# Kernel optimization log

Hardware: AMD Instinct MI355X
Metric: run time of the kernel (lower is better)

The kernel has to match this reference:

```python
import jax, jax.numpy as jnp
import numpy as np


def setup_inputs() -> dict:
    key = jax.random.key(0)
    k1, k2, k3, k4 = jax.random.split(key, 4)
    B, S, D, R = 8, 1024, 1024, 256
    batch = jax.random.normal(k1, (B, S, D), dtype=jnp.float32)
    proj_L = jax.random.uniform(k2, (D, R), dtype=jnp.float32, minval=-0.05, maxval=0.05)
    proj_R = jax.random.uniform(k3, (R, D), dtype=jnp.float32, minval=-0.05, maxval=0.05)
    bias = jax.random.uniform(k4, (1,), dtype=jnp.float32, minval=-0.05, maxval=0.05)
    return {"batch": batch, "proj_L": proj_L, "proj_R": proj_R, "bias": bias}


def reference(batch, proj_L, proj_R, bias):
    # logits[b,i,j] = h_i^T (L @ R) h_j + bias
    # Efficient factored form (same math, avoids O(B*S^2*D) intermediates):
    # left[b,i,r] = (batch @ L)[b,i,r]; right[b,j,r] = (batch @ R^T)[b,j,r]
    left = jnp.einsum('bid,dr->bir', batch, proj_L)    # (B,S,R)
    right = jnp.einsum('bjd,rd->bjr', batch, proj_R)   # (B,S,R)
    logits = jnp.einsum('bir,bjr->bij', left, right) + bias[0]
    return logits
```

## Files before the change

### kernel.cpp

```cpp
#include <hip/hip_runtime.h>

typedef __bf16 bf16_t;
typedef __bf16 bf16x8 __attribute__((ext_vector_type(8)));
typedef __bf16 bf16x4 __attribute__((ext_vector_type(4)));
typedef float f32x4 __attribute__((ext_vector_type(4)));

__device__ __forceinline__ void async16(const void* g, void* l) {
  __builtin_amdgcn_global_load_lds(
      (const __attribute__((address_space(1))) unsigned int*)g,
      (__attribute__((address_space(3))) unsigned int*)l,
      16, 0, 0);
}

__global__ void convert_f32_bf16(const float* __restrict__ in,
                                 bf16_t* __restrict__ out, int n4) {
  int i = blockIdx.x * blockDim.x + threadIdx.x;
  if (i >= n4) return;
  float4 v = ((const float4*)in)[i];
  bf16x4 o;
  o[0] = (bf16_t)v.x; o[1] = (bf16_t)v.y; o[2] = (bf16_t)v.z; o[3] = (bf16_t)v.w;
  ((bf16x4*)out)[i] = o;
}

__global__ void transpose_L(const float* __restrict__ in,
                            bf16_t* __restrict__ out) {
  __shared__ float tile[32][33];
  const int n0 = blockIdx.x * 32;
  const int k0 = blockIdx.y * 32;
  const int tx = threadIdx.x;
  const int ty = threadIdx.y;
#pragma unroll
  for (int i = 0; i < 32; i += 8)
    tile[ty + i][tx] = in[(long)(k0 + ty + i) * 256 + n0 + tx];
  __syncthreads();
#pragma unroll
  for (int i = 0; i < 32; i += 8)
    out[(long)(n0 + ty + i) * 1024 + k0 + tx] = (bf16_t)tile[tx][ty + i];
}

template <bool BF16_OUT>
__global__ __launch_bounds__(256) void gemm_bt(
    const bf16_t* __restrict__ A0, long sA, int lda,
    const bf16_t* __restrict__ B0, long sB, int ldb,
    void* __restrict__ C0, long sC, int ldc,
    int K, int tilesN, const float* __restrict__ bias) {
  const int bz = blockIdx.y;
  const bf16_t* A = A0 + (long)bz * sA;
  const bf16_t* Bt = B0 + (long)bz * sB;
  const int tm = (int)(blockIdx.x / tilesN) * 128;
  const int tn = (int)(blockIdx.x % tilesN) * 128;

  __shared__ __attribute__((aligned(16))) bf16_t As[128 * 32];
  __shared__ __attribute__((aligned(16))) bf16_t Bs[128 * 32];

  const int t = threadIdx.x;
  const int lane = t & 63;
  const int quad = lane >> 4;
  const int l15 = lane & 15;
  const int wave = t >> 6;
  const int wr = (wave >> 1) * 64;
  const int wc = (wave & 1) * 64;

  const int rS = t >> 2;
  const int cS = (t & 3) * 8;
  const bf16_t* gA = A + (long)(tm + rS) * lda + cS;
  const bf16_t* gB = Bt + (long)(tn + rS) * ldb + cS;
  bf16_t* lA = As + t * 8;
  bf16_t* lB = Bs + t * 8;

  f32x4 acc[4][4];
#pragma unroll
  for (int i = 0; i < 4; ++i)
#pragma unroll
    for (int j = 0; j < 4; ++j)
      acc[i][j] = (f32x4){0.f, 0.f, 0.f, 0.f};

  for (int k0 = 0; k0 < K; k0 += 32) {
    async16(gA + k0, lA);
    async16(gA + k0 + (long)64 * lda, lA + 2048);
    async16(gB + k0, lB);
    async16(gB + k0 + (long)64 * ldb, lB + 2048);
    __syncthreads();

    bf16x8 af[4], bv[4];
#pragma unroll
    for (int i = 0; i < 4; ++i)
      af[i] = *(const bf16x8*)(As + (wr + i * 16 + l15) * 32 + quad * 8);
#pragma unroll
    for (int j = 0; j < 4; ++j)
      bv[j] = *(const bf16x8*)(Bs + (wc + j * 16 + l15) * 32 + quad * 8);
#pragma unroll
    for (int i = 0; i < 4; ++i)
#pragma unroll
      for (int j = 0; j < 4; ++j)
        acc[i][j] = __builtin_amdgcn_mfma_f32_16x16x32_bf16(af[i], bv[j],
                                                            acc[i][j], 0, 0, 0);
    __syncthreads();
  }

  if constexpr (BF16_OUT) {
    bf16_t* C = (bf16_t*)C0 + (long)bz * sC;
#pragma unroll
    for (int i = 0; i < 4; ++i) {
      const int r0 = tm + wr + i * 16 + quad * 4;
#pragma unroll
      for (int j = 0; j < 4; ++j) {
        const int c0 = tn + wc + j * 16 + l15;
#pragma unroll
        for (int r = 0; r < 4; ++r)
          C[(long)(r0 + r) * ldc + c0] = (bf16_t)acc[i][j][r];
      }
    }
  } else {
    float* C = (float*)C0 + (long)bz * sC;
    const float bvadd = bias[0];
#pragma unroll
    for (int i = 0; i < 4; ++i) {
      const int r0 = tm + wr + i * 16 + quad * 4;
#pragma unroll
      for (int j = 0; j < 4; ++j) {
        const int c0 = tn + wc + j * 16 + l15;
#pragma unroll
        for (int r = 0; r < 4; ++r)
          C[(long)(r0 + r) * ldc + c0] = acc[i][j][r] + bvadd;
      }
    }
  }
}

extern "C" void kernel_launch(void* const* d_in, const int* in_sizes, int n_in,
                              void* d_out, int out_size, void* d_ws,
                              size_t ws_size, hipStream_t stream) {
  const float* batch = (const float*)d_in[0];
  const float* projL = (const float*)d_in[1];
  const float* projR = (const float*)d_in[2];
  const float* bias = (const float*)d_in[3];
  float* out = (float*)d_out;

  constexpr int B = 8, S = 1024, D = 1024, R = 256;
  constexpr long nBatch = (long)B * S * D;

  char* ws = (char*)d_ws;
  bf16_t* batch_bf = (bf16_t*)ws;
  bf16_t* Bcat = (bf16_t*)(ws + nBatch * 2);
  bf16_t* LR = (bf16_t*)(ws + nBatch * 2 + (long)512 * 1024 * 2);

  convert_f32_bf16<<<(int)(nBatch / 4 + 255) / 256, 256, 0, stream>>>(
      batch, batch_bf, (int)(nBatch / 4));
  convert_f32_bf16<<<(R * D / 4 + 255) / 256, 256, 0, stream>>>(
      projR, Bcat + (long)256 * 1024, R * D / 4);
  transpose_L<<<dim3(8, 32), dim3(32, 8), 0, stream>>>(projL, Bcat);

  gemm_bt<true><<<dim3(64 * 4, 1), 256, 0, stream>>>(
      batch_bf, 0L, D, Bcat, 0L, D, (void*)LR, 0L, 512, D, 4, nullptr);

  gemm_bt<false><<<dim3(8 * 8, 8), 256, 0, stream>>>(
      LR, (long)S * 512, 512, LR + 256, (long)S * 512, 512, (void*)out,
      (long)S * S, S, R, 8, bias);
}
```

Before: 134.7 us.

## Load four K-chunks per barrier in GEMM and merge weight prep kernels

The GEMM main loop now stages four 32-wide K slices (128 total) into LDS before each barrier pair, which cuts the number of __syncthreads and gives the async loads more in flight. LDS use per block grows fourfold, to 64 KB, which may lower occupancy. Separately, the projR conversion and the projL transpose are merged into a single launch, saving one kernel launch. The second GEMM has K=256, so it runs only two iterations of the new loop.

Result: faster. 123.0 us (-8.7%).

```diff
diff --git a/kernel.cpp b/kernel.cpp
--- a/kernel.cpp
+++ b/kernel.cpp
@@ -22,20 +22,31 @@
   ((bf16x4*)out)[i] = o;
 }
 
-__global__ void transpose_L(const float* __restrict__ in,
-                            bf16_t* __restrict__ out) {
-  __shared__ float tile[32][33];
-  const int n0 = blockIdx.x * 32;
-  const int k0 = blockIdx.y * 32;
-  const int tx = threadIdx.x;
-  const int ty = threadIdx.y;
+__global__ void prep_Bcat(const float* __restrict__ projL,
+                          const float* __restrict__ projR,
+                          bf16_t* __restrict__ Bcat) {
+  const int t = threadIdx.x;
+  if (blockIdx.x < 256) {
+    int i = blockIdx.x * 256 + t;
+    float4 v = ((const float4*)projR)[i];
+    bf16x4 o;
+    o[0] = (bf16_t)v.x; o[1] = (bf16_t)v.y; o[2] = (bf16_t)v.z; o[3] = (bf16_t)v.w;
+    ((bf16x4*)(Bcat + (long)256 * 1024))[i] = o;
+  } else {
+    __shared__ float tile[32][33];
+    const int bb = blockIdx.x - 256;
+    const int n0 = (bb & 7) * 32;
+    const int k0 = (bb >> 3) * 32;
+    const int tx = t & 31;
+    const int ty = t >> 5;
 #pragma unroll
-  for (int i = 0; i < 32; i += 8)
-    tile[ty + i][tx] = in[(long)(k0 + ty + i) * 256 + n0 + tx];
-  __syncthreads();
+    for (int i = 0; i < 32; i += 8)
+      tile[ty + i][tx] = projL[(long)(k0 + ty + i) * 256 + n0 + tx];
+    __syncthreads();
 #pragma unroll
-  for (int i = 0; i < 32; i += 8)
-    out[(long)(n0 + ty + i) * 1024 + k0 + tx] = (bf16_t)tile[tx][ty + i];
+    for (int i = 0; i < 32; i += 8)
+      Bcat[(long)(n0 + ty + i) * 1024 + k0 + tx] = (bf16_t)tile[tx][ty + i];
+  }
 }
 
 template <bool BF16_OUT>
@@ -50,8 +61,8 @@
   const int tm = (int)(blockIdx.x / tilesN) * 128;
   const int tn = (int)(blockIdx.x % tilesN) * 128;
 
-  __shared__ __attribute__((aligned(16))) bf16_t As[128 * 32];
-  __shared__ __attribute__((aligned(16))) bf16_t Bs[128 * 32];
+  __shared__ __attribute__((aligned(16))) bf16_t As[4 * 128 * 32];
+  __shared__ __attribute__((aligned(16))) bf16_t Bs[4 * 128 * 32];
 
   const int t = threadIdx.x;
   const int lane = t & 63;
@@ -75,26 +86,36 @@
     for (int j = 0; j < 4; ++j)
       acc[i][j] = (f32x4){0.f, 0.f, 0.f, 0.f};
 
-  for (int k0 = 0; k0 < K; k0 += 32) {
-    async16(gA + k0, lA);
-    async16(gA + k0 + (long)64 * lda, lA + 2048);
-    async16(gB + k0, lB);
-    async16(gB + k0 + (long)64 * ldb, lB + 2048);
+  for (int k0 = 0; k0 < K; k0 += 128) {
+#pragma unroll
+    for (int kc = 0; kc < 4; ++kc) {
+      const int ko = k0 + kc * 32;
+      const int lo = kc * 4096;
+      async16(gA + ko, lA + lo);
+      async16(gA + ko + (long)64 * lda, lA + lo + 2048);
+      async16(gB + ko, lB + lo);
+      async16(gB + ko + (long)64 * ldb, lB + lo + 2048);
+    }
     __syncthreads();
 
-    bf16x8 af[4], bv[4];
 #pragma unroll
-    for (int i = 0; i < 4; ++i)
-      af[i] = *(const bf16x8*)(As + (wr + i * 16 + l15) * 32 + quad * 8);
+    for (int kc = 0; kc < 4; ++kc) {
+      const bf16_t* Ak = As + kc * 4096;
+      const bf16_t* Bk = Bs + kc * 4096;
+      bf16x8 af[4], bv[4];
 #pragma unroll
-    for (int j = 0; j < 4; ++j)
-      bv[j] = *(const bf16x8*)(Bs + (wc + j * 16 + l15) * 32 + quad * 8);
-#pragma unroll
-    for (int i = 0; i < 4; ++i)
+      for (int i = 0; i < 4; ++i)
+        af[i] = *(const bf16x8*)(Ak + (wr + i * 16 + l15) * 32 + quad * 8);
 #pragma unroll
       for (int j = 0; j < 4; ++j)
-        acc[i][j] = __builtin_amdgcn_mfma_f32_16x16x32_bf16(af[i], bv[j],
-                                                            acc[i][j], 0, 0, 0);
+        bv[j] = *(const bf16x8*)(Bk + (wc + j * 16 + l15) * 32 + quad * 8);
+#pragma unroll
+      for (int i = 0; i < 4; ++i)
+#pragma unroll
+        for (int j = 0; j < 4; ++j)
+          acc[i][j] = __builtin_amdgcn_mfma_f32_16x16x32_bf16(af[i], bv[j],
+                                                              acc[i][j], 0, 0, 0);
+    }
     __syncthreads();
   }
 
@@ -147,9 +168,7 @@
 
   convert_f32_bf16<<<(int)(nBatch / 4 + 255) / 256, 256, 0, stream>>>(
       batch, batch_bf, (int)(nBatch / 4));
-  convert_f32_bf16<<<(R * D / 4 + 255) / 256, 256, 0, stream>>>(
-      projR, Bcat + (long)256 * 1024, R * D / 4);
-  transpose_L<<<dim3(8, 32), dim3(32, 8), 0, stream>>>(projL, Bcat);
+  prep_Bcat<<<512, 256, 0, stream>>>(projL, projR, Bcat);
 
   gemm_bt<true><<<dim3(64 * 4, 1), 256, 0, stream>>>(
       batch_bf, 0L, D, Bcat, 0L, D, (void*)LR, 0L, 512, D, 4, nullptr);
```
